# Optimization experiments

Measured on AMD Instinct MI355X. Metric: run time of the kernel, lower is better.

The kernel has to match this reference:

```python
import jax, jax.numpy as jnp
import numpy as np

B = 2048
D = 256  # manifold_dim == rank (required for the perturbation add to broadcast)
NUM_CHARTS = 4


def setup_inputs() -> dict:
    key = jax.random.key(0)
    k1, k2 = jax.random.split(key)
    x = jax.random.normal(k1, (B, D), dtype=jnp.float32)
    metric_factors = jax.random.normal(k2, (NUM_CHARTS, D, D), dtype=jnp.float32)
    return {"x": x, "metric_factors": metric_factors, "chart": 0}


def reference(x, metric_factors, chart):
    # x: [B, D]; metric_factors: [num_charts, rank, D] with rank == D
    d = x.shape[-1]
    factors = metric_factors[chart]                      # [D, D]
    perturbation = factors @ factors.T                   # [D, D]
    # Fisher-Rao term. In the original loops:
    #   fisher[b,i,j] = sum_k p[b,k]*(1-p[b,k]) * x[b,i] * x[b,j]
    # which factors into an outer product scaled by s[b] = sum_k p(1-p).
    probs = jax.nn.softmax(x, axis=-1)                   # [B, D]
    s = jnp.sum(probs * (1.0 - probs), axis=-1)          # [B]
    fisher = s[:, None, None] * (x[:, :, None] * x[:, None, :])  # [B, D, D]
    base = jnp.eye(d, dtype=x.dtype)[None] + perturbation[None]  # [1, D, D]
    return base + fisher
```

## Files before the change

### kernel.cpp

```cpp
#include <hip/hip_runtime.h>
#include <math.h>


#define DIM 256
#define BATCH 2048

__global__ __launch_bounds__(256) void base_kernel(const float* __restrict__ mf,
                                                   const int* __restrict__ chart,
                                                   float* __restrict__ base) {
    const float* F = mf + (size_t)chart[0] * DIM * DIM;
    __shared__ float As[32][33];
    __shared__ float Bs[32][33];
    const int tx = threadIdx.x, ty = threadIdx.y;
    const int tid = ty * 16 + tx;
    const int i0 = blockIdx.y * 32, j0 = blockIdx.x * 32;
    float acc00 = 0.f, acc01 = 0.f, acc10 = 0.f, acc11 = 0.f;

    const int lrow = tid >> 3;
    const int lc4  = (tid & 7) * 4;

    for (int k0 = 0; k0 < DIM; k0 += 32) {
        float4 a = *(const float4*)(F + (size_t)(i0 + lrow) * DIM + k0 + lc4);
        float4 b = *(const float4*)(F + (size_t)(j0 + lrow) * DIM + k0 + lc4);
        As[lrow][lc4 + 0] = a.x; As[lrow][lc4 + 1] = a.y;
        As[lrow][lc4 + 2] = a.z; As[lrow][lc4 + 3] = a.w;
        Bs[lrow][lc4 + 0] = b.x; Bs[lrow][lc4 + 1] = b.y;
        Bs[lrow][lc4 + 2] = b.z; Bs[lrow][lc4 + 3] = b.w;
        __syncthreads();
        #pragma unroll
        for (int kk = 0; kk < 32; ++kk) {
            float a0 = As[ty * 2 + 0][kk];
            float a1 = As[ty * 2 + 1][kk];
            float b0 = Bs[tx * 2 + 0][kk];
            float b1 = Bs[tx * 2 + 1][kk];
            acc00 += a0 * b0; acc01 += a0 * b1;
            acc10 += a1 * b0; acc11 += a1 * b1;
        }
        __syncthreads();
    }
    const int i = i0 + ty * 2, j = j0 + tx * 2;
    base[(size_t)(i + 0) * DIM + (j + 0)] = acc00 + ((i + 0) == (j + 0) ? 1.0f : 0.0f);
    base[(size_t)(i + 0) * DIM + (j + 1)] = acc01 + ((i + 0) == (j + 1) ? 1.0f : 0.0f);
    base[(size_t)(i + 1) * DIM + (j + 0)] = acc10 + ((i + 1) == (j + 0) ? 1.0f : 0.0f);
    base[(size_t)(i + 1) * DIM + (j + 1)] = acc11 + ((i + 1) == (j + 1) ? 1.0f : 0.0f);
}

__global__ __launch_bounds__(256) void main_kernel(const float* __restrict__ x,
                                                   const float* __restrict__ base,
                                                   float* __restrict__ out) {
    const int b = blockIdx.x;
    const int t = threadIdx.x;
    __shared__ float xs[DIM];
    __shared__ float redm[4], redz[4], redq[4];
    __shared__ float bmax_sh, s_sh;

    const float xv = x[(size_t)b * DIM + t];
    xs[t] = xv;

    float m = xv;
    #pragma unroll
    for (int off = 32; off; off >>= 1) m = fmaxf(m, __shfl_xor(m, off));
    const int wave = t >> 6;
    if ((t & 63) == 0) redm[wave] = m;
    __syncthreads();
    if (t == 0) bmax_sh = fmaxf(fmaxf(redm[0], redm[1]), fmaxf(redm[2], redm[3]));
    __syncthreads();
    m = bmax_sh;

    const float e = __expf(xv - m);
    float z = e, q = e * e;
    #pragma unroll
    for (int off = 32; off; off >>= 1) { z += __shfl_xor(z, off); q += __shfl_xor(q, off); }
    if ((t & 63) == 0) { redz[wave] = z; redq[wave] = q; }
    __syncthreads();
    if (t == 0) {
        float Z = redz[0] + redz[1] + redz[2] + redz[3];
        float Q = redq[0] + redq[1] + redq[2] + redq[3];
        s_sh = 1.0f - Q / (Z * Z);
    }
    __syncthreads();
    const float s = s_sh;

    const float4* xs4   = (const float4*)xs;
    const float4* base4 = (const float4*)base;
    float4* out4 = (float4*)(out + (size_t)b * DIM * DIM);

    const int j4   = t & 63;
    const int irow = t >> 6;
    const float4 xj = xs4[j4];

    #pragma unroll 4
    for (int it = 0; it < 64; ++it) {
        const int i = it * 4 + irow;
        const float sx = s * xs[i];
        const float4 bb = base4[i * 64 + j4];
        float4 v;
        v.x = bb.x + sx * xj.x;
        v.y = bb.y + sx * xj.y;
        v.z = bb.z + sx * xj.z;
        v.w = bb.w + sx * xj.w;
        out4[i * 64 + j4] = v;
    }
}

extern "C" void kernel_launch(void* const* d_in, const int* in_sizes, int n_in,
                              void* d_out, int out_size, void* d_ws, size_t ws_size,
                              hipStream_t stream) {
    const float* x  = (const float*)d_in[0];
    const float* mf = (const float*)d_in[1];
    const int* chart = (const int*)d_in[2];
    float* out  = (float*)d_out;
    float* base = (float*)d_ws;

    base_kernel<<<dim3(8, 8), dim3(16, 16), 0, stream>>>(mf, chart, base);
    main_kernel<<<dim3(BATCH), dim3(256), 0, stream>>>(x, base, out);
}
```

Before: 538.9 us.

## Split softmax stats into own kernel and tile main kernel with register-resident base

Moves the per-row softmax statistic s into a separate wave-per-row kernel. The main kernel is retiled so each block handles 16 batch rows by 32 output rows and keeps its base slice in registers, which stops re-reading the full base matrix for every batch element. Output writes use nontemporal stores to avoid polluting the cache with the large write-only output. This adds an extra kernel launch and a dependency on s in workspace.

Result: no change. 539.8 us (+0.2%).

```diff
diff --git a/kernel.cpp b/kernel.cpp
--- a/kernel.cpp
+++ b/kernel.cpp
@@ -4,6 +4,10 @@
 
 #define DIM 256
 #define BATCH 2048
+#define NB 16
+#define RB 32
+
+typedef float f4 __attribute__((ext_vector_type(4)));
 
 __global__ __launch_bounds__(256) void base_kernel(const float* __restrict__ mf,
                                                    const int* __restrict__ chart,
@@ -45,61 +49,65 @@
     base[(size_t)(i + 1) * DIM + (j + 1)] = acc11 + ((i + 1) == (j + 1) ? 1.0f : 0.0f);
 }
 
+__global__ __launch_bounds__(256) void s_kernel(const float* __restrict__ x,
+                                                float* __restrict__ s) {
+    const int row  = blockIdx.x * 4 + (threadIdx.x >> 6);
+    const int lane = threadIdx.x & 63;
+    const float4 v = *(const float4*)(x + (size_t)row * DIM + lane * 4);
+    float m = fmaxf(fmaxf(v.x, v.y), fmaxf(v.z, v.w));
+    #pragma unroll
+    for (int off = 32; off; off >>= 1) m = fmaxf(m, __shfl_xor(m, off));
+    const float e0 = __expf(v.x - m), e1 = __expf(v.y - m);
+    const float e2 = __expf(v.z - m), e3 = __expf(v.w - m);
+    float z = e0 + e1 + e2 + e3;
+    float q = e0 * e0 + e1 * e1 + e2 * e2 + e3 * e3;
+    #pragma unroll
+    for (int off = 32; off; off >>= 1) { z += __shfl_xor(z, off); q += __shfl_xor(q, off); }
+    if (lane == 0) s[row] = 1.0f - q / (z * z);
+}
+
 __global__ __launch_bounds__(256) void main_kernel(const float* __restrict__ x,
+                                                   const float* __restrict__ s,
                                                    const float* __restrict__ base,
                                                    float* __restrict__ out) {
-    const int b = blockIdx.x;
-    const int t = threadIdx.x;
-    __shared__ float xs[DIM];
-    __shared__ float redm[4], redz[4], redq[4];
-    __shared__ float bmax_sh, s_sh;
+    const int t  = threadIdx.x;
+    const int b0 = blockIdx.x * NB;
+    const int i0 = blockIdx.y * RB;
 
-    const float xv = x[(size_t)b * DIM + t];
-    xs[t] = xv;
+    __shared__ float xs[NB][DIM];
+    __shared__ float sxs[NB][RB];
 
-    float m = xv;
+    f4 breg[8];
+    const f4* base4 = (const f4*)(base + (size_t)i0 * DIM);
     #pragma unroll
-    for (int off = 32; off; off >>= 1) m = fmaxf(m, __shfl_xor(m, off));
-    const int wave = t >> 6;
-    if ((t & 63) == 0) redm[wave] = m;
-    __syncthreads();
-    if (t == 0) bmax_sh = fmaxf(fmaxf(redm[0], redm[1]), fmaxf(redm[2], redm[3]));
-    __syncthreads();
-    m = bmax_sh;
+    for (int k = 0; k < 8; ++k) breg[k] = base4[k * 256 + t];
 
-    const float e = __expf(xv - m);
-    float z = e, q = e * e;
+    {
+        const f4* xg = (const f4*)(x + (size_t)b0 * DIM);
+        f4* xl = (f4*)xs;
+        #pragma unroll
+        for (int k = 0; k < 4; ++k) xl[k * 256 + t] = xg[k * 256 + t];
+    }
     #pragma unroll
-    for (int off = 32; off; off >>= 1) { z += __shfl_xor(z, off); q += __shfl_xor(q, off); }
-    if ((t & 63) == 0) { redz[wave] = z; redq[wave] = q; }
-    __syncthreads();
-    if (t == 0) {
-        float Z = redz[0] + redz[1] + redz[2] + redz[3];
-        float Q = redq[0] + redq[1] + redq[2] + redq[3];
-        s_sh = 1.0f - Q / (Z * Z);
+    for (int k = 0; k < 2; ++k) {
+        const int lin = k * 256 + t;
+        const int bb = lin >> 5, r = lin & 31;
+        sxs[bb][r] = s[b0 + bb] * x[(size_t)(b0 + bb) * DIM + i0 + r];
     }
     __syncthreads();
-    const float s = s_sh;
 
-    const float4* xs4   = (const float4*)xs;
-    const float4* base4 = (const float4*)base;
-    float4* out4 = (float4*)(out + (size_t)b * DIM * DIM);
+    const int irow = t >> 6, j4 = t & 63;
+    float* outp = out + (size_t)b0 * DIM * DIM + (size_t)i0 * DIM;
 
-    const int j4   = t & 63;
-    const int irow = t >> 6;
-    const float4 xj = xs4[j4];
-
-    #pragma unroll 4
-    for (int it = 0; it < 64; ++it) {
-        const int i = it * 4 + irow;
-        const float sx = s * xs[i];
-        const float4 bb = base4[i * 64 + j4];
-        float4 v;
-        v.x = bb.x + sx * xj.x;
-        v.y = bb.y + sx * xj.y;
-        v.z = bb.z + sx * xj.z;
-        v.w = bb.w + sx * xj.w;
-        out4[i * 64 + j4] = v;
+    for (int b = 0; b < NB; ++b) {
+        const f4 xj = ((const f4*)xs[b])[j4];
+        f4* o4 = (f4*)(outp + (size_t)b * DIM * DIM);
+        #pragma unroll
+        for (int k = 0; k < 8; ++k) {
+            const float sxv = sxs[b][k * 4 + irow];
+            f4 v = breg[k] + sxv * xj;
+            __builtin_nontemporal_store(v, o4 + (k * 4 + irow) * 64 + j4);
+        }
     }
 }
 
@@ -111,7 +119,9 @@
     const int* chart = (const int*)d_in[2];
     float* out  = (float*)d_out;
     float* base = (float*)d_ws;
+    float* s    = base + DIM * DIM;
 
     base_kernel<<<dim3(8, 8), dim3(16, 16), 0, stream>>>(mf, chart, base);
-    main_kernel<<<dim3(BATCH), dim3(256), 0, stream>>>(x, base, out);
+    s_kernel<<<dim3(BATCH / 4), dim3(256), 0, stream>>>(x, s);
+    main_kernel<<<dim3(BATCH / NB, DIM / RB), dim3(256), 0, stream>>>(x, s, base, out);
 }
```
